# Kernel optimization log

Hardware: AMD Instinct MI355X
Metric: run time of the kernel (lower is better)

The kernel has to match this reference:

```python
import jax, jax.numpy as jnp
import numpy as np

N_NODES = 50000
N_EDGES = 800000
IN_DIM = 64
EDGE_DIM = 16
HID = 128
L = 3
G = 128  # number of graphs in the batch
EPS = 1e-5


def _glorot(key, shape):
    fan_in, fan_out = shape[0], shape[1]
    lim = float(np.sqrt(6.0 / (fan_in + fan_out)))
    return jax.random.uniform(key, shape, jnp.float32, -lim, lim)


def setup_inputs() -> dict:
    key = jax.random.key(0)
    ks = jax.random.split(key, 40)
    inp = {}
    inp["x"] = jax.random.uniform(ks[0], (N_NODES, IN_DIM), jnp.float32)
    inp["edge_index"] = jax.random.randint(ks[1], (2, N_EDGES), 0, N_NODES, jnp.int64)
    inp["edge_attr"] = jax.random.normal(ks[2], (N_EDGES, EDGE_DIM), jnp.float32)
    inp["batch"] = jnp.sort(jax.random.randint(ks[3], (N_NODES,), 0, G, jnp.int64))
    # ligand / protein input MLPs: Linear-ReLU-Linear-ReLU
    inp["lig_w1"] = _glorot(ks[4], (IN_DIM, HID)); inp["lig_b1"] = jnp.zeros((HID,), jnp.float32)
    inp["lig_w2"] = _glorot(ks[5], (HID, HID));    inp["lig_b2"] = jnp.zeros((HID,), jnp.float32)
    inp["prot_w1"] = _glorot(ks[6], (IN_DIM, HID)); inp["prot_b1"] = jnp.zeros((HID,), jnp.float32)
    inp["prot_w2"] = _glorot(ks[7], (HID, HID));    inp["prot_b2"] = jnp.zeros((HID,), jnp.float32)
    # per-layer GINEConv params (stacked over layers)
    inp["edge_w"] = jnp.stack([_glorot(ks[8 + i], (EDGE_DIM, HID)) for i in range(L)])
    inp["edge_b"] = jnp.zeros((L, HID), jnp.float32)
    inp["nn_w1"] = jnp.stack([_glorot(ks[12 + i], (HID, HID)) for i in range(L)])
    inp["nn_b1"] = jnp.zeros((L, HID), jnp.float32)
    inp["nn_w2"] = jnp.stack([_glorot(ks[16 + i], (HID, HID)) for i in range(L)])
    inp["nn_b2"] = jnp.zeros((L, HID), jnp.float32)
    # GraphNorm params: weight=1, bias=0, mean_scale=1
    inp["gn_w"] = jnp.ones((L, HID), jnp.float32)
    inp["gn_b"] = jnp.zeros((L, HID), jnp.float32)
    inp["gn_ms"] = jnp.ones((L, HID), jnp.float32)
    # output head: Linear-ReLU-Linear(1)
    inp["fc_w1"] = _glorot(ks[20], (HID, HID)); inp["fc_b1"] = jnp.zeros((HID,), jnp.float32)
    inp["fc_w2"] = _glorot(ks[21], (HID, 1));   inp["fc_b2"] = jnp.zeros((1,), jnp.float32)
    return inp


def reference(x, edge_index, edge_attr, batch,
              lig_w1, lig_b1, lig_w2, lig_b2,
              prot_w1, prot_b1, prot_w2, prot_b2,
              edge_w, edge_b, nn_w1, nn_b1, nn_w2, nn_b2,
              gn_w, gn_b, gn_ms,
              fc_w1, fc_b1, fc_w2, fc_b2):
    relu = lambda a: jnp.maximum(a, 0)
    src, dst = edge_index[0], edge_index[1]

    # input encoders, merged per node by protein flag (last feature column)
    is_prot = x[:, -1] > 0.5
    h_lig = relu(relu(x @ lig_w1 + lig_b1) @ lig_w2 + lig_b2)
    h_prot = relu(relu(x @ prot_w1 + prot_b1) @ prot_w2 + prot_b2)
    h = jnp.where(is_prot[:, None], h_prot, h_lig)

    # per-graph node counts for GraphNorm
    cnt = jax.ops.segment_sum(jnp.ones((x.shape[0],), jnp.float32), batch, num_segments=G)
    cnt = jnp.maximum(cnt, 1.0)[:, None]

    for l in range(L):
        # GINEConv (eps=0): out = nn(x + sum_{j->i} relu(x_j + lin(e_ji)))
        e = edge_attr @ edge_w[l] + edge_b[l]              # [E, HID]
        msg = relu(h[src] + e)                             # gather + add + relu
        aggr = jax.ops.segment_sum(msg, dst, num_segments=h.shape[0])
        h = aggr + h
        h = relu(h @ nn_w1[l] + nn_b1[l]) @ nn_w2[l] + nn_b2[l]
        # GraphNorm: per-graph mean/var with learnable mean_scale
        mean = jax.ops.segment_sum(h, batch, num_segments=G) / cnt
        hc = h - mean[batch] * gn_ms[l]
        var = jax.ops.segment_sum(hc * hc, batch, num_segments=G) / cnt
        h = gn_w[l] * hc * jax.lax.rsqrt(var[batch] + EPS) + gn_b[l]
        h = relu(h)  # (dropout=0.0 -> identity)

    g = jax.ops.segment_sum(h, batch, num_segments=G)      # global_add_pool
    out = relu(g @ fc_w1 + fc_b1) @ fc_w2 + fc_b2
    return out.reshape(-1)
```

## Files before the change

kernel.cpp:

```cpp
#include <hip/hip_runtime.h>

#define N_NODES 50000
#define N_EDGES 800000
#define IN_DIM  64
#define EDGE_DIM 16
#define HID     128
#define NLAYERS 3
#define NGRAPH  128
#define EPS     1e-5f

typedef __attribute__((ext_vector_type(8))) short bf8_t;
typedef __attribute__((ext_vector_type(4))) float f32x4;

__device__ __forceinline__ unsigned short f2bf(float x) {
    unsigned u = __float_as_uint(x);
    unsigned r = u + 0x7fffu + ((u >> 16) & 1u);
    return (unsigned short)(r >> 16);
}

__global__ void k_init(int* __restrict__ row_cnt, float* __restrict__ pool,
                       float* __restrict__ gsum, float* __restrict__ gsq) {
    int i = blockIdx.x * blockDim.x + threadIdx.x;
    if (i < N_NODES) row_cnt[i] = 0;
    if (i < NGRAPH * HID) { pool[i] = 0.0f; gsum[i] = 0.0f; gsq[i] = 0.0f; }
}

__global__ __launch_bounds__(NGRAPH) void k_count(const int* __restrict__ batch,
                                                  float* __restrict__ cnt) {
    int g = threadIdx.x;
    int lo = 0, hi = N_NODES;
    while (lo < hi) { int mid = (lo + hi) >> 1; if (batch[mid] < g) lo = mid + 1; else hi = mid; }
    int a = lo;
    lo = 0; hi = N_NODES;
    while (lo < hi) { int mid = (lo + hi) >> 1; if (batch[mid] < g + 1) lo = mid + 1; else hi = mid; }
    cnt[g] = (float)(lo - a);
}

__global__ void k_wconv(const float* __restrict__ nw1, const float* __restrict__ nw2,
                        unsigned short* __restrict__ wt) {
    int idx = blockIdx.x * 256 + threadIdx.x;
    if (idx >= NLAYERS * 2 * HID * HID) return;
    int k = idx & 127;
    int n = (idx >> 7) & 127;
    int which = (idx >> 14) & 1;
    int l = idx >> 15;
    const float* w = (which == 0 ? nw1 : nw2) + l * HID * HID;
    wt[idx] = f2bf(w[k * HID + n]);
}

__global__ void k_wconv_enc(const float* __restrict__ lw1, const float* __restrict__ pw1,
                            const float* __restrict__ lw2, const float* __restrict__ pw2,
                            unsigned short* __restrict__ we) {
    int idx = blockIdx.x * 256 + threadIdx.x;
    if (idx >= 49152) return;
    float v;
    if (idx < 8192)       { int n = idx >> 6, k = idx & 63;            v = lw1[k * HID + n]; }
    else if (idx < 16384) { int r = idx - 8192;  int n = r >> 6, k = r & 63;  v = pw1[k * HID + n]; }
    else if (idx < 32768) { int r = idx - 16384; int n = r >> 7, k = r & 127; v = lw2[k * HID + n]; }
    else                  { int r = idx - 32768; int n = r >> 7, k = r & 127; v = pw2[k * HID + n]; }
    we[idx] = f2bf(v);
}

__global__ void k_wconv_e(const float* __restrict__ ew, unsigned short* __restrict__ wte) {
    int idx = blockIdx.x * 256 + threadIdx.x;
    if (idx >= NLAYERS * 8 * 64 * 8) return;
    int j = idx & 7;
    int lane = (idx >> 3) & 63;
    int t = (idx >> 9) & 7;
    int l = idx >> 12;
    int k = (lane >> 4) * 8 + j;
    int feat = t * 16 + (lane & 15);
    float v = (k < EDGE_DIM) ? ew[l * EDGE_DIM * HID + k * HID + feat] : 0.0f;
    wte[idx] = f2bf(v);
}

__global__ void k_hist(const int* __restrict__ dsts, int* __restrict__ row_cnt) {
    int e = blockIdx.x * blockDim.x + threadIdx.x;
    if (e < N_EDGES) atomicAdd(&row_cnt[dsts[e]], 1);
}

__global__ __launch_bounds__(256) void k_scan1(const int* __restrict__ row_cnt,
                                               int* __restrict__ partial) {
    __shared__ int s[256];
    int t = threadIdx.x, b = blockIdx.x;
    int i0 = b * 512 + t;
    int v = 0;
    if (i0 < N_NODES) v += row_cnt[i0];
    if (i0 + 256 < N_NODES) v += row_cnt[i0 + 256];
    s[t] = v; __syncthreads();
    for (int off = 128; off > 0; off >>= 1) {
        if (t < off) s[t] += s[t + off];
        __syncthreads();
    }
    if (t == 0) partial[b] = s[0];
}

#define NCHUNK 98
__global__ __launch_bounds__(128) void k_scan2(int* __restrict__ partial) {
    __shared__ int s[128];
    int t = threadIdx.x;
    int v = (t < NCHUNK) ? partial[t] : 0;
    s[t] = v; __syncthreads();
    for (int off = 1; off < 128; off <<= 1) {
        int x = (t >= off) ? s[t - off] : 0;
        __syncthreads();
        s[t] += x;
        __syncthreads();
    }
    partial[t] = s[t] - v;
}

__global__ __launch_bounds__(512) void k_scan3(const int* __restrict__ row_cnt,
                                               const int* __restrict__ partial,
                                               int* __restrict__ row_start,
                                               int* __restrict__ row_fill) {
    __shared__ int s[512];
    int t = threadIdx.x, b = blockIdx.x;
    int i = b * 512 + t;
    int v = (i < N_NODES) ? row_cnt[i] : 0;
    s[t] = v; __syncthreads();
    for (int off = 1; off < 512; off <<= 1) {
        int x = (t >= off) ? s[t - off] : 0;
        __syncthreads();
        s[t] += x;
        __syncthreads();
    }
    int excl = s[t] - v + partial[b];
    if (i < N_NODES) { row_start[i] = excl; row_fill[i] = excl; }
}

__global__ void k_fill(const int* __restrict__ srcs, const int* __restrict__ dsts,
                       const float* __restrict__ ea,
                       int* __restrict__ row_fill,
                       int* __restrict__ csr_src, unsigned short* __restrict__ cea) {
    int e = blockIdx.x * blockDim.x + threadIdx.x;
    if (e < N_EDGES) {
        int p = atomicAdd(&row_fill[dsts[e]], 1);
        csr_src[p] = srcs[e];
        const float* s = ea + (size_t)e * EDGE_DIM;
        bf8_t v0, v1;
        #pragma unroll
        for (int k = 0; k < 8; ++k) v0[k] = (short)f2bf(s[k]);
        #pragma unroll
        for (int k = 0; k < 8; ++k) v1[k] = (short)f2bf(s[8 + k]);
        *(bf8_t*)(cea + (size_t)p * EDGE_DIM) = v0;
        *(bf8_t*)(cea + (size_t)p * EDGE_DIM + 8) = v1;
    }
}

#define HS 136
__global__ __launch_bounds__(256) void k_encoder_mfma(
    const float* __restrict__ x,
    const unsigned short* __restrict__ we,
    const float* __restrict__ lb1, const float* __restrict__ lb2,
    const float* __restrict__ pb1, const float* __restrict__ pb2,
    float* __restrict__ H) {
    __shared__ short h1l[4 * 16 * HS];
    __shared__ short h1p[4 * 16 * HS];
    int w = threadIdx.x >> 6, lane = threadIdx.x & 63;
    int m = lane & 15, quad = lane >> 4;
    int nb = blockIdx.x * 64 + w * 16;
    short* hl = h1l + w * 16 * HS;
    short* hp = h1p + w * 16 * HS;
    int nclamp = nb + m; if (nclamp >= N_NODES) nclamp = N_NODES - 1;
    const float* xp = x + (size_t)nclamp * IN_DIM;

    f32x4 a1l[8], a1p[8];
    #pragma unroll
    for (int t = 0; t < 8; ++t) {
        float bl = lb1[t * 16 + m], bp = pb1[t * 16 + m];
        a1l[t] = (f32x4){bl, bl, bl, bl};
        a1p[t] = (f32x4){bp, bp, bp, bp};
    }
    #pragma unroll
    for (int s_ = 0; s_ < 2; ++s_) {
        int k0 = s_ * 32 + quad * 8;
        float4 a0 = *(const float4*)(xp + k0);
        float4 a1v = *(const float4*)(xp + k0 + 4);
        bf8_t af;
        af[0] = (short)f2bf(a0.x); af[1] = (short)f2bf(a0.y);
        af[2] = (short)f2bf(a0.z); af[3] = (short)f2bf(a0.w);
        af[4] = (short)f2bf(a1v.x); af[5] = (short)f2bf(a1v.y);
        af[6] = (short)f2bf(a1v.z); af[7] = (short)f2bf(a1v.w);
        #pragma unroll
        for (int t = 0; t < 8; ++t) {
            bf8_t bl = *(const bf8_t*)(we + (t * 16 + m) * 64 + k0);
            bf8_t bp = *(const bf8_t*)(we + 8192 + (t * 16 + m) * 64 + k0);
            a1l[t] = __builtin_amdgcn_mfma_f32_16x16x32_bf16(af, bl, a1l[t], 0, 0, 0);
            a1p[t] = __builtin_amdgcn_mfma_f32_16x16x32_bf16(af, bp, a1p[t], 0, 0, 0);
        }
    }
    #pragma unroll
    for (int t = 0; t < 8; ++t)
        #pragma unroll
        for (int r = 0; r < 4; ++r) {
            hl[(quad * 4 + r) * HS + t * 16 + m] = (short)f2bf(fmaxf(a1l[t][r], 0.0f));
            hp[(quad * 4 + r) * HS + t * 16 + m] = (short)f2bf(fmaxf(a1p[t][r], 0.0f));
        }
    __syncthreads();
    f32x4 a2l[8], a2p[8];
    #pragma unroll
    for (int t = 0; t < 8; ++t) {
        float bl = lb2[t * 16 + m], bp = pb2[t * 16 + m];
        a2l[t] = (f32x4){bl, bl, bl, bl};
        a2p[t] = (f32x4){bp, bp, bp, bp};
    }
    #pragma unroll
    for (int s_ = 0; s_ < 4; ++s_) {
        int k0 = s_ * 32 + quad * 8;
        bf8_t afl = *(const bf8_t*)(hl + m * HS + k0);
        bf8_t afp = *(const bf8_t*)(hp + m * HS + k0);
        #pragma unroll
        for (int t = 0; t < 8; ++t) {
            bf8_t bl = *(const bf8_t*)(we + 16384 + (t * 16 + m) * 128 + k0);
            bf8_t bp = *(const bf8_t*)(we + 32768 + (t * 16 + m) * 128 + k0);
            a2l[t] = __builtin_amdgcn_mfma_f32_16x16x32_bf16(afl, bl, a2l[t], 0, 0, 0);
            a2p[t] = __builtin_amdgcn_mfma_f32_16x16x32_bf16(afp, bp, a2p[t], 0, 0, 0);
        }
    }
    float flg[4];
    #pragma unroll
    for (int r = 0; r < 4; ++r) {
        int node = nb + quad * 4 + r; if (node >= N_NODES) node = N_NODES - 1;
        flg[r] = x[(size_t)node * IN_DIM + (IN_DIM - 1)];
    }
    #pragma unroll
    for (int t = 0; t < 8; ++t)
        #pragma unroll
        for (int r = 0; r < 4; ++r) {
            int node = nb + quad * 4 + r;
            if (node < N_NODES) {
                float v = (flg[r] > 0.5f) ? a2p[t][r] : a2l[t][r];
                H[(size_t)node * HID + t * 16 + m] = fmaxf(v, 0.0f);
            }
        }
}

__global__ __launch_bounds__(256) void k_gather(
    const int* __restrict__ csr_src, const unsigned short* __restrict__ cea,
    const int* __restrict__ row_start, const int* __restrict__ row_end,
    const unsigned short* __restrict__ wte, const float* __restrict__ eb,
    const float* __restrict__ H, float* __restrict__ A) {
    int w = threadIdx.x >> 6, lane = threadIdx.x & 63;
    int m = lane & 15, quad = lane >> 4;
    int n = blockIdx.x * 4 + w;
    bf8_t bw[8];
    #pragma unroll
    for (int t = 0; t < 8; ++t)
        bw[t] = *(const bf8_t*)(wte + ((size_t)t * 64 + lane) * 8);
    float ebv[8];
    #pragma unroll
    for (int t = 0; t < 8; ++t) ebv[t] = eb[t * 16 + m];
    float acc[8];
    #pragma unroll
    for (int t = 0; t < 8; ++t) acc[t] = 0.0f;

    int p  = __builtin_amdgcn_readfirstlane(row_start[n]);
    int pe = __builtin_amdgcn_readfirstlane(row_end[n]);

    for (; p + 16 <= pe; p += 16) {
        bf8_t af = (bf8_t){0, 0, 0, 0, 0, 0, 0, 0};
        if (quad < 2)
            af = *(const bf8_t*)(cea + (size_t)(p + m) * EDGE_DIM + quad * 8);
        int sr[4];
        #pragma unroll
        for (int r = 0; r < 4; ++r) sr[r] = csr_src[p + quad * 4 + r];
        float h[8][4];
        #pragma unroll
        for (int r = 0; r < 4; ++r) {
            const float* hb = H + (size_t)sr[r] * HID + m;
            #pragma unroll
            for (int t = 0; t < 8; ++t) h[t][r] = hb[t * 16];
        }
        f32x4 d[8];
        #pragma unroll
        for (int t = 0; t < 8; ++t)
            d[t] = __builtin_amdgcn_mfma_f32_16x16x32_bf16(
                af, bw[t], (f32x4){ebv[t], ebv[t], ebv[t], ebv[t]}, 0, 0, 0);
        #pragma unroll
        for (int t = 0; t < 8; ++t)
            #pragma unroll
            for (int r = 0; r < 4; ++r)
                acc[t] += fmaxf(h[t][r] + d[t][r], 0.0f);
    }
    int rem = pe - p;
    if (rem > 0) {
        bf8_t af = (bf8_t){0, 0, 0, 0, 0, 0, 0, 0};
        if (quad < 2 && m < rem)
            af = *(const bf8_t*)(cea + (size_t)(p + m) * EDGE_DIM + quad * 8);
        int sr[4];
        #pragma unroll
        for (int r = 0; r < 4; ++r) {
            int idx = p + quad * 4 + r; if (idx >= pe) idx = pe - 1;
            sr[r] = csr_src[idx];
        }
        float h[8][4];
        #pragma unroll
        for (int r = 0; r < 4; ++r) {
            const float* hb = H + (size_t)sr[r] * HID + m;
            #pragma unroll
            for (int t = 0; t < 8; ++t) h[t][r] = hb[t * 16];
        }
        f32x4 d[8];
        #pragma unroll
        for (int t = 0; t < 8; ++t)
            d[t] = __builtin_amdgcn_mfma_f32_16x16x32_bf16(
                af, bw[t], (f32x4){ebv[t], ebv[t], ebv[t], ebv[t]}, 0, 0, 0);
        #pragma unroll
        for (int t = 0; t < 8; ++t)
            #pragma unroll
            for (int r = 0; r < 4; ++r)
                if (quad * 4 + r < rem) acc[t] += fmaxf(h[t][r] + d[t][r], 0.0f);
    }
    #pragma unroll
    for (int t = 0; t < 8; ++t) {
        acc[t] += __shfl_xor(acc[t], 16);
        acc[t] += __shfl_xor(acc[t], 32);
    }
    int t0 = quad * 2, t1 = quad * 2 + 1;
    size_t base = (size_t)n * HID;
    A[base + t0 * 16 + m] = acc[t0] + H[base + t0 * 16 + m];
    A[base + t1 * 16 + m] = acc[t1] + H[base + t1 * 16 + m];
}

#define MLP_NODES_PER_BLOCK 64
__global__ __launch_bounds__(256) void k_mlp_mfma(
    const float* __restrict__ A, const int* __restrict__ batch,
    const unsigned short* __restrict__ wt1, const unsigned short* __restrict__ wt2,
    const float* __restrict__ b1, const float* __restrict__ b2,
    float* __restrict__ H, float* __restrict__ gsum, float* __restrict__ gsq) {
    __shared__ short h1s[4 * 16 * HS];
    int w = threadIdx.x >> 6;
    int lane = threadIdx.x & 63;
    int m = lane & 15;
    int quad = lane >> 4;
    int nb = blockIdx.x * MLP_NODES_PER_BLOCK + w * 16;
    short* hw = h1s + w * 16 * HS;

    int nclamp = nb + m; if (nclamp >= N_NODES) nclamp = N_NODES - 1;
    const float* Ap = A + (size_t)nclamp * HID;
    f32x4 acc1[8];
    #pragma unroll
    for (int t = 0; t < 8; ++t) {
        float bv = b1[t * 16 + m];
        acc1[t] = (f32x4){bv, bv, bv, bv};
    }
    #pragma unroll
    for (int s_ = 0; s_ < 4; ++s_) {
        int k0 = s_ * 32 + quad * 8;
        float4 a0 = *(const float4*)(Ap + k0);
        float4 a1 = *(const float4*)(Ap + k0 + 4);
        bf8_t af;
        af[0] = (short)f2bf(a0.x); af[1] = (short)f2bf(a0.y);
        af[2] = (short)f2bf(a0.z); af[3] = (short)f2bf(a0.w);
        af[4] = (short)f2bf(a1.x); af[5] = (short)f2bf(a1.y);
        af[6] = (short)f2bf(a1.z); af[7] = (short)f2bf(a1.w);
        #pragma unroll
        for (int t = 0; t < 8; ++t) {
            bf8_t bf = *(const bf8_t*)(wt1 + (t * 16 + m) * HID + k0);
            acc1[t] = __builtin_amdgcn_mfma_f32_16x16x32_bf16(af, bf, acc1[t], 0, 0, 0);
        }
    }
    #pragma unroll
    for (int t = 0; t < 8; ++t)
        #pragma unroll
        for (int r = 0; r < 4; ++r) {
            float v = fmaxf(acc1[t][r], 0.0f);
            hw[(quad * 4 + r) * HS + t * 16 + m] = (short)f2bf(v);
        }
    __syncthreads();
    f32x4 acc2[8];
    #pragma unroll
    for (int t = 0; t < 8; ++t) {
        float bv = b2[t * 16 + m];
        acc2[t] = (f32x4){bv, bv, bv, bv};
    }
    #pragma unroll
    for (int s_ = 0; s_ < 4; ++s_) {
        int k0 = s_ * 32 + quad * 8;
        bf8_t af = *(const bf8_t*)(hw + m * HS + k0);
        #pragma unroll
        for (int t = 0; t < 8; ++t) {
            bf8_t bf = *(const bf8_t*)(wt2 + (t * 16 + m) * HID + k0);
            acc2[t] = __builtin_amdgcn_mfma_f32_16x16x32_bf16(af, bf, acc2[t], 0, 0, 0);
        }
    }
    #pragma unroll
    for (int t = 0; t < 8; ++t)
        #pragma unroll
        for (int r = 0; r < 4; ++r) {
            int node = nb + quad * 4 + r;
            if (node < N_NODES) H[(size_t)node * HID + t * 16 + m] = acc2[t][r];
        }
    int blast = nb + 15 < N_NODES ? batch[nb + 15] : -1;
    int g0 = batch[nb < N_NODES ? nb : N_NODES - 1];
    if (nb + 15 < N_NODES && g0 == blast) {
        #pragma unroll
        for (int t = 0; t < 8; ++t) {
            float s = 0.0f, q = 0.0f;
            #pragma unroll
            for (int r = 0; r < 4; ++r) { float v = acc2[t][r]; s += v; q += v * v; }
            s += __shfl_xor(s, 16); q += __shfl_xor(q, 16);
            s += __shfl_xor(s, 32); q += __shfl_xor(q, 32);
            if (quad == 0) {
                atomicAdd(&gsum[g0 * HID + t * 16 + m], s);
                atomicAdd(&gsq[g0 * HID + t * 16 + m], q);
            }
        }
    } else {
        #pragma unroll
        for (int t = 0; t < 8; ++t)
            #pragma unroll
            for (int r = 0; r < 4; ++r) {
                int node = nb + quad * 4 + r;
                if (node < N_NODES) {
                    int g = batch[node];
                    float v = acc2[t][r];
                    atomicAdd(&gsum[g * HID + t * 16 + m], v);
                    atomicAdd(&gsq[g * HID + t * 16 + m], v * v);
                }
            }
    }
}

__global__ __launch_bounds__(HID) void k_stats(
    float* __restrict__ gsum, float* __restrict__ gsq,
    const float* __restrict__ cnt,
    const float* __restrict__ gw, const float* __restrict__ gb,
    const float* __restrict__ gms,
    float* __restrict__ sc, float* __restrict__ of) {
    int g = blockIdx.x;
    int t = threadIdx.x;
    float c = fmaxf(cnt[g], 1.0f);
    float mean = gsum[g * HID + t] / c;
    float msq  = gsq[g * HID + t] / c;
    float ms = gms[t];
    float var = msq - mean * mean * ms * (2.0f - ms);
    var = fmaxf(var, 0.0f);
    float istd = rsqrtf(var + EPS);
    float s = gw[t] * istd;
    sc[g * HID + t] = s;
    of[g * HID + t] = gb[t] - s * mean * ms;
    gsum[g * HID + t] = 0.0f;
    gsq[g * HID + t]  = 0.0f;
}

#define NORM_N 8
__global__ __launch_bounds__(HID) void k_norm(
    float* __restrict__ H, const int* __restrict__ batch,
    const float* __restrict__ sc, const float* __restrict__ of,
    float* __restrict__ pool, int accumulate) {
    int n0 = blockIdx.x * NORM_N;
    int t = threadIdx.x;
    int g0 = batch[n0], gN = batch[n0 + NORM_N - 1];
    if (g0 == gN) {
        float ssc = sc[g0 * HID + t], sof = of[g0 * HID + t];
        float ps = 0.0f;
        #pragma unroll
        for (int i = 0; i < NORM_N; ++i) {
            float v = fmaxf(H[(n0 + i) * HID + t] * ssc + sof, 0.0f);
            H[(n0 + i) * HID + t] = v;
            ps += v;
        }
        if (accumulate) atomicAdd(&pool[g0 * HID + t], ps);
    } else {
        #pragma unroll
        for (int i = 0; i < NORM_N; ++i) {
            int g = batch[n0 + i];
            float v = fmaxf(H[(n0 + i) * HID + t] * sc[g * HID + t] + of[g * HID + t], 0.0f);
            H[(n0 + i) * HID + t] = v;
            if (accumulate) atomicAdd(&pool[g * HID + t], v);
        }
    }
}

__global__ __launch_bounds__(HID) void k_head(
    const float* __restrict__ pool,
    const float* __restrict__ fw1, const float* __restrict__ fb1,
    const float* __restrict__ fw2, const float* __restrict__ fb2,
    float* __restrict__ out) {
    __shared__ float ps[HID];
    __shared__ float red[2];
    int g = blockIdx.x;
    int t = threadIdx.x;
    ps[t] = pool[g * HID + t];
    __syncthreads();
    float acc = fb1[t];
    #pragma unroll 4
    for (int k = 0; k < HID; ++k) acc = fmaf(ps[k], fw1[k * HID + t], acc);
    float p = fmaxf(acc, 0.0f) * fw2[t];
    #pragma unroll
    for (int off = 32; off > 0; off >>= 1) p += __shfl_down(p, off, 64);
    if ((t & 63) == 0) red[t >> 6] = p;
    __syncthreads();
    if (t == 0) out[g] = red[0] + red[1] + fb2[0];
}

extern "C" void kernel_launch(void* const* d_in, const int* in_sizes, int n_in,
                              void* d_out, int out_size, void* d_ws, size_t ws_size,
                              hipStream_t stream) {
    const float* x     = (const float*)d_in[0];
    const int*   ei    = (const int*)d_in[1];
    const float* ea    = (const float*)d_in[2];
    const int*   batch = (const int*)d_in[3];
    const float* lw1 = (const float*)d_in[4];
    const float* lb1 = (const float*)d_in[5];
    const float* lw2 = (const float*)d_in[6];
    const float* lb2 = (const float*)d_in[7];
    const float* pw1 = (const float*)d_in[8];
    const float* pb1 = (const float*)d_in[9];
    const float* pw2 = (const float*)d_in[10];
    const float* pb2 = (const float*)d_in[11];
    const float* ew  = (const float*)d_in[12];
    const float* eb  = (const float*)d_in[13];
    const float* nw1 = (const float*)d_in[14];
    const float* nb1 = (const float*)d_in[15];
    const float* nw2 = (const float*)d_in[16];
    const float* nb2 = (const float*)d_in[17];
    const float* gw  = (const float*)d_in[18];
    const float* gb  = (const float*)d_in[19];
    const float* gms = (const float*)d_in[20];
    const float* fw1 = (const float*)d_in[21];
    const float* fb1 = (const float*)d_in[22];
    const float* fw2 = (const float*)d_in[23];
    const float* fb2 = (const float*)d_in[24];
    float* out = (float*)d_out;

    float* ws   = (float*)d_ws;
    float* H    = ws;
    float* A    = H    + (size_t)N_NODES * HID;
    float* gsum = A    + (size_t)N_NODES * HID;
    float* gsq  = gsum + NGRAPH * HID;
    float* sc   = gsq  + NGRAPH * HID;
    float* of   = sc   + NGRAPH * HID;
    float* pool = of   + NGRAPH * HID;
    float* cnt  = pool + NGRAPH * HID;
    int* row_cnt   = (int*)(cnt + NGRAPH);
    int* row_start = row_cnt + N_NODES;
    int* row_fill  = row_start + N_NODES;
    int* partial   = row_fill + N_NODES;
    int* csr_src   = partial + 128;
    unsigned short* cea  = (unsigned short*)(csr_src + N_EDGES);
    unsigned short* wt   = cea + (size_t)N_EDGES * EDGE_DIM;
    unsigned short* wenc = wt + NLAYERS * 2 * HID * HID;
    unsigned short* wte  = wenc + 49152;

    const int* srcs = ei;
    const int* dsts = ei + N_EDGES;

    k_init<<<(N_NODES + 255) / 256, 256, 0, stream>>>(row_cnt, pool, gsum, gsq);
    k_count<<<1, NGRAPH, 0, stream>>>(batch, cnt);
    k_wconv<<<(NLAYERS * 2 * HID * HID + 255) / 256, 256, 0, stream>>>(nw1, nw2, wt);
    k_wconv_enc<<<(49152 + 255) / 256, 256, 0, stream>>>(lw1, pw1, lw2, pw2, wenc);
    k_wconv_e<<<(NLAYERS * 8 * 64 * 8 + 255) / 256, 256, 0, stream>>>(ew, wte);
    k_hist<<<(N_EDGES + 255) / 256, 256, 0, stream>>>(dsts, row_cnt);
    k_scan1<<<NCHUNK, 256, 0, stream>>>(row_cnt, partial);
    k_scan2<<<1, 128, 0, stream>>>(partial);
    k_scan3<<<NCHUNK, 512, 0, stream>>>(row_cnt, partial, row_start, row_fill);
    k_fill<<<(N_EDGES + 255) / 256, 256, 0, stream>>>(srcs, dsts, ea, row_fill,
                                                      csr_src, cea);

    k_encoder_mfma<<<(N_NODES + 63) / 64, 256, 0, stream>>>(
        x, wenc, lb1, lb2, pb1, pb2, H);

    int mlp_blocks = (N_NODES + MLP_NODES_PER_BLOCK - 1) / MLP_NODES_PER_BLOCK;
    for (int l = 0; l < NLAYERS; ++l) {
        k_gather<<<N_NODES / 4, 256, 0, stream>>>(
            csr_src, cea, row_start, row_fill,
            wte + (size_t)l * 4096, eb + l * HID, H, A);
        k_mlp_mfma<<<mlp_blocks, 256, 0, stream>>>(
            A, batch,
            wt + (size_t)l * 2 * HID * HID,
            wt + (size_t)l * 2 * HID * HID + HID * HID,
            nb1 + l * HID, nb2 + l * HID, H, gsum, gsq);
        k_stats<<<NGRAPH, HID, 0, stream>>>(gsum, gsq, cnt,
                                            gw + l * HID, gb + l * HID, gms + l * HID,
                                            sc, of);
        k_norm<<<N_NODES / NORM_N, HID, 0, stream>>>(
            H, batch, sc, of, pool, (l == NLAYERS - 1) ? 1 : 0);
    }
    k_head<<<NGRAPH, HID, 0, stream>>>(pool, fw1, fb1, fw2, fb2, out);
}
```

Before: 735.3 us.

## Store node features as interleaved bf16 for the edge gather

The encoder and the norm kernel now write node features as bf16 in a permuted layout, with each lane's 8 features packed contiguously. The gather kernel reads one 16-byte vector per source node instead of eight strided fp32 loads. This halves the bytes moved by the random-access gather, which dominates the layer cost, and cuts the number of load instructions. In exchange, features are rounded to bf16 before aggregation, which adds a small error.

```diff
diff --git a/kernel.cpp b/kernel.cpp
--- a/kernel.cpp
+++ b/kernel.cpp
@@ -16,6 +16,9 @@
     unsigned u = __float_as_uint(x);
     unsigned r = u + 0x7fffu + ((u >> 16) & 1u);
     return (unsigned short)(r >> 16);
+}
+__device__ __forceinline__ float bf2f(unsigned short v) {
+    return __uint_as_float(((unsigned)v) << 16);
 }
 
 __global__ void k_init(int* __restrict__ row_cnt, float* __restrict__ pool,
@@ -154,7 +157,7 @@
     const unsigned short* __restrict__ we,
     const float* __restrict__ lb1, const float* __restrict__ lb2,
     const float* __restrict__ pb1, const float* __restrict__ pb2,
-    float* __restrict__ H) {
+    unsigned short* __restrict__ Hbp) {
     __shared__ short h1l[4 * 16 * HS];
     __shared__ short h1p[4 * 16 * HS];
     int w = threadIdx.x >> 6, lane = threadIdx.x & 63;
@@ -218,29 +221,28 @@
             a2p[t] = __builtin_amdgcn_mfma_f32_16x16x32_bf16(afp, bp, a2p[t], 0, 0, 0);
         }
     }
-    float flg[4];
     #pragma unroll
     for (int r = 0; r < 4; ++r) {
-        int node = nb + quad * 4 + r; if (node >= N_NODES) node = N_NODES - 1;
-        flg[r] = x[(size_t)node * IN_DIM + (IN_DIM - 1)];
-    }
-    #pragma unroll
-    for (int t = 0; t < 8; ++t)
-        #pragma unroll
-        for (int r = 0; r < 4; ++r) {
-            int node = nb + quad * 4 + r;
-            if (node < N_NODES) {
-                float v = (flg[r] > 0.5f) ? a2p[t][r] : a2l[t][r];
-                H[(size_t)node * HID + t * 16 + m] = fmaxf(v, 0.0f);
+        int node = nb + quad * 4 + r;
+        if (node < N_NODES) {
+            float flg = x[(size_t)node * IN_DIM + (IN_DIM - 1)];
+            bool prot = flg > 0.5f;
+            bf8_t o;
+            #pragma unroll
+            for (int t = 0; t < 8; ++t) {
+                float v = prot ? a2p[t][r] : a2l[t][r];
+                o[t] = (short)f2bf(fmaxf(v, 0.0f));
             }
-        }
+            *(bf8_t*)(Hbp + (size_t)node * HID + m * 8) = o;
+        }
+    }
 }
 
 __global__ __launch_bounds__(256) void k_gather(
     const int* __restrict__ csr_src, const unsigned short* __restrict__ cea,
     const int* __restrict__ row_start, const int* __restrict__ row_end,
     const unsigned short* __restrict__ wte, const float* __restrict__ eb,
-    const float* __restrict__ H, float* __restrict__ A) {
+    const unsigned short* __restrict__ Hbp, float* __restrict__ A) {
     int w = threadIdx.x >> 6, lane = threadIdx.x & 63;
     int m = lane & 15, quad = lane >> 4;
     int n = blockIdx.x * 4 + w;
@@ -265,13 +267,10 @@
         int sr[4];
         #pragma unroll
         for (int r = 0; r < 4; ++r) sr[r] = csr_src[p + quad * 4 + r];
-        float h[8][4];
-        #pragma unroll
-        for (int r = 0; r < 4; ++r) {
-            const float* hb = H + (size_t)sr[r] * HID + m;
-            #pragma unroll
-            for (int t = 0; t < 8; ++t) h[t][r] = hb[t * 16];
-        }
+        bf8_t hrow[4];
+        #pragma unroll
+        for (int r = 0; r < 4; ++r)
+            hrow[r] = *(const bf8_t*)(Hbp + (size_t)sr[r] * HID + m * 8);
         f32x4 d[8];
         #pragma unroll
         for (int t = 0; t < 8; ++t)
@@ -281,7 +280,7 @@
         for (int t = 0; t < 8; ++t)
             #pragma unroll
             for (int r = 0; r < 4; ++r)
-                acc[t] += fmaxf(h[t][r] + d[t][r], 0.0f);
+                acc[t] += fmaxf(bf2f((unsigned short)hrow[r][t]) + d[t][r], 0.0f);
     }
     int rem = pe - p;
     if (rem > 0) {
@@ -294,13 +293,10 @@
             int idx = p + quad * 4 + r; if (idx >= pe) idx = pe - 1;
             sr[r] = csr_src[idx];
         }
-        float h[8][4];
-        #pragma unroll
-        for (int r = 0; r < 4; ++r) {
-            const float* hb = H + (size_t)sr[r] * HID + m;
-            #pragma unroll
-            for (int t = 0; t < 8; ++t) h[t][r] = hb[t * 16];
-        }
+        bf8_t hrow[4];
+        #pragma unroll
+        for (int r = 0; r < 4; ++r)
+            hrow[r] = *(const bf8_t*)(Hbp + (size_t)sr[r] * HID + m * 8);
         f32x4 d[8];
         #pragma unroll
         for (int t = 0; t < 8; ++t)
@@ -310,7 +306,8 @@
         for (int t = 0; t < 8; ++t)
             #pragma unroll
             for (int r = 0; r < 4; ++r)
-                if (quad * 4 + r < rem) acc[t] += fmaxf(h[t][r] + d[t][r], 0.0f);
+                if (quad * 4 + r < rem)
+                    acc[t] += fmaxf(bf2f((unsigned short)hrow[r][t]) + d[t][r], 0.0f);
     }
     #pragma unroll
     for (int t = 0; t < 8; ++t) {
@@ -318,9 +315,12 @@
         acc[t] += __shfl_xor(acc[t], 32);
     }
     int t0 = quad * 2, t1 = quad * 2 + 1;
+    const unsigned short* selfp = Hbp + (size_t)n * HID + m * 8;
+    float s0 = bf2f(selfp[t0]);
+    float s1 = bf2f(selfp[t1]);
     size_t base = (size_t)n * HID;
-    A[base + t0 * 16 + m] = acc[t0] + H[base + t0 * 16 + m];
-    A[base + t1 * 16 + m] = acc[t1] + H[base + t1 * 16 + m];
+    A[base + t0 * 16 + m] = acc[t0] + s0;
+    A[base + t1 * 16 + m] = acc[t1] + s1;
 }
 
 #define MLP_NODES_PER_BLOCK 64
@@ -447,19 +447,20 @@
 
 #define NORM_N 8
 __global__ __launch_bounds__(HID) void k_norm(
-    float* __restrict__ H, const int* __restrict__ batch,
+    const float* __restrict__ H, const int* __restrict__ batch,
     const float* __restrict__ sc, const float* __restrict__ of,
-    float* __restrict__ pool, int accumulate) {
+    unsigned short* __restrict__ Hbp, float* __restrict__ pool, int accumulate) {
     int n0 = blockIdx.x * NORM_N;
     int t = threadIdx.x;
+    int m = t & 15, tt = t >> 4;
     int g0 = batch[n0], gN = batch[n0 + NORM_N - 1];
     if (g0 == gN) {
         float ssc = sc[g0 * HID + t], sof = of[g0 * HID + t];
         float ps = 0.0f;
         #pragma unroll
         for (int i = 0; i < NORM_N; ++i) {
-            float v = fmaxf(H[(n0 + i) * HID + t] * ssc + sof, 0.0f);
-            H[(n0 + i) * HID + t] = v;
+            float v = fmaxf(H[(size_t)(n0 + i) * HID + t] * ssc + sof, 0.0f);
+            Hbp[(size_t)(n0 + i) * HID + m * 8 + tt] = f2bf(v);
             ps += v;
         }
         if (accumulate) atomicAdd(&pool[g0 * HID + t], ps);
@@ -467,8 +468,8 @@
         #pragma unroll
         for (int i = 0; i < NORM_N; ++i) {
             int g = batch[n0 + i];
-            float v = fmaxf(H[(n0 + i) * HID + t] * sc[g * HID + t] + of[g * HID + t], 0.0f);
-            H[(n0 + i) * HID + t] = v;
+            float v = fmaxf(H[(size_t)(n0 + i) * HID + t] * sc[g * HID + t] + of[g * HID + t], 0.0f);
+            Hbp[(size_t)(n0 + i) * HID + m * 8 + tt] = f2bf(v);
             if (accumulate) atomicAdd(&pool[g * HID + t], v);
         }
     }
@@ -544,6 +545,7 @@
     unsigned short* wt   = cea + (size_t)N_EDGES * EDGE_DIM;
     unsigned short* wenc = wt + NLAYERS * 2 * HID * HID;
     unsigned short* wte  = wenc + 49152;
+    unsigned short* Hbp  = wte + NLAYERS * 8 * 64 * 8;
 
     const int* srcs = ei;
     const int* dsts = ei + N_EDGES;
@@ -561,13 +563,13 @@
                                                       csr_src, cea);
 
     k_encoder_mfma<<<(N_NODES + 63) / 64, 256, 0, stream>>>(
-        x, wenc, lb1, lb2, pb1, pb2, H);
+        x, wenc, lb1, lb2, pb1, pb2, Hbp);
 
     int mlp_blocks = (N_NODES + MLP_NODES_PER_BLOCK - 1) / MLP_NODES_PER_BLOCK;
     for (int l = 0; l < NLAYERS; ++l) {
         k_gather<<<N_NODES / 4, 256, 0, stream>>>(
             csr_src, cea, row_start, row_fill,
-            wte + (size_t)l * 4096, eb + l * HID, H, A);
+            wte + (size_t)l * 4096, eb + l * HID, Hbp, A);
         k_mlp_mfma<<<mlp_blocks, 256, 0, stream>>>(
             A, batch,
             wt + (size_t)l * 2 * HID * HID,
@@ -577,7 +579,7 @@
                                             gw + l * HID, gb + l * HID, gms + l * HID,
                                             sc, of);
         k_norm<<<N_NODES / NORM_N, HID, 0, stream>>>(
-            H, batch, sc, of, pool, (l == NLAYERS - 1) ? 1 : 0);
+            H, batch, sc, of, Hbp, pool, (l == NLAYERS - 1) ? 1 : 0);
     }
     k_head<<<NGRAPH, HID, 0, stream>>>(pool, fw1, fb1, fw2, fb2, out);
 }
```

Result: faster. 707.1 us (-3.8%).
